# Optimization experiments

Hardware: AMD Instinct MI355X
Metric: run time of the kernel (lower is better)

## Reference

```python
import jax, jax.numpy as jnp
import numpy as np

HID = 512      # hidden_dim
MID = 256      # hid_dim
COND_D = 256   # condition_op_dim
OP_D = 32      # operator_len
EX_D = 32      # extra_info_num
L, N, T = 16, 1024, 8
EPS = 1e-5


def _lstm_cell(x_proj, h, c, Whh, bhh):
    # x_proj: precomputed x @ Wih.T + bih, shape [B, 4H]
    gates = x_proj + h @ Whh.T + bhh
    i, f, g, o = jnp.split(gates, 4, axis=-1)
    i = jax.nn.sigmoid(i); f = jax.nn.sigmoid(f)
    g = jnp.tanh(g); o = jax.nn.sigmoid(o)
    c = f * c + i * g
    h = o * jnp.tanh(c)
    return h, c


def _batchnorm(x, gamma, beta):
    mu = x.mean(0)
    var = x.var(0)  # biased, matches PyTorch training-mode normalization
    return gamma * (x - mu) * jax.lax.rsqrt(var + EPS) + beta


def setup_inputs() -> dict:
    key = jax.random.key(0)
    ks = jax.random.split(key, 24)
    s = lambda *sh: 0.05
    inp = {
        'operators': jax.random.normal(ks[0], (L, N, OP_D), jnp.float32),
        'extra_infos': jax.random.normal(ks[1], (L, N, EX_D), jnp.float32),
        'conditions': jax.random.normal(ks[2], (L, N, T, COND_D), jnp.float32),
        'condition_masks': jnp.ones((L, N, 1), jnp.float32),
        'mapping': jax.random.randint(ks[3], (L, N, 2), 0, N + 1, jnp.int32).astype(jnp.int64),
        'lstm1_Wih': jax.random.normal(ks[4], (4 * HID, COND_D), jnp.float32) * 0.05,
        'lstm1_Whh': jax.random.normal(ks[5], (4 * HID, HID), jnp.float32) * 0.05,
        'lstm1_bih': jnp.zeros((4 * HID,), jnp.float32),
        'lstm1_bhh': jnp.zeros((4 * HID,), jnp.float32),
        'cond_W': jax.random.normal(ks[6], (MID, HID), jnp.float32) * 0.05,
        'cond_b': jnp.zeros((MID,), jnp.float32),
        'bn1_g': jnp.ones((MID,), jnp.float32),
        'bn1_b': jnp.zeros((MID,), jnp.float32),
        'lstm2_Wih': jax.random.normal(ks[7], (4 * HID, OP_D + EX_D + MID), jnp.float32) * 0.05,
        'lstm2_Whh': jax.random.normal(ks[8], (4 * HID, HID), jnp.float32) * 0.05,
        'lstm2_bih': jnp.zeros((4 * HID,), jnp.float32),
        'lstm2_bhh': jnp.zeros((4 * HID,), jnp.float32),
        'bn2_g': jnp.ones((HID,), jnp.float32),
        'bn2_b': jnp.zeros((HID,), jnp.float32),
    }
    return inp


def reference(operators, extra_infos, conditions, condition_masks, mapping,
              lstm1_Wih, lstm1_Whh, lstm1_bih, lstm1_bhh,
              cond_W, cond_b, bn1_g, bn1_b,
              lstm2_Wih, lstm2_Whh, lstm2_bih, lstm2_bhh,
              bn2_g, bn2_b):
    B = L * N
    x = conditions.reshape(B, T, COND_D)
    # lstm1 over conditions; precompute input projections for all steps
    xp = jnp.einsum('btd,gd->btg', x, lstm1_Wih) + lstm1_bih  # [B,T,4H]

    def step1(carry, xt):
        h, c = carry
        h, c = _lstm_cell(xt, h, c, lstm1_Whh, lstm1_bhh)
        return (h, c), None

    h0 = jnp.zeros((B, HID), xp.dtype)
    (h1, _), _ = jax.lax.scan(step1, (h0, h0), jnp.swapaxes(xp, 0, 1))

    last = jax.nn.relu(h1 @ cond_W.T + cond_b)       # [B, MID]
    last = _batchnorm(last, bn1_g, bn1_b).reshape(L, N, MID)

    out = jnp.concatenate([operators, extra_infos, last], axis=2)  # [L,N,IN2]
    xp2 = jnp.einsum('lnd,gd->lng', out, lstm2_Wih) + lstm2_bih    # [L,N,4H]

    hz = jnp.zeros((N, HID), xp2.dtype)
    h, c = _lstm_cell(xp2[L - 1], hz, hz, lstm2_Whh, lstm2_bhh)

    mapping = mapping.astype(jnp.int32)
    levels = jnp.arange(L - 2, -1, -1)

    def tree_step(carry, idx):
        h, c = carry
        mp = mapping[idx]  # [N,2]
        pad = jnp.zeros((1, HID), h.dtype)
        ph = jnp.concatenate([pad, h], 0)  # [N+1,H]
        pc = jnp.concatenate([pad, c], 0)
        h = (ph[mp[:, 0]] + ph[mp[:, 1]]) * 0.5
        c = (pc[mp[:, 0]] + pc[mp[:, 1]]) * 0.5
        h, c = _lstm_cell(xp2[idx], h, c, lstm2_Whh, lstm2_bhh)
        return (h, c), None

    (h, c), _ = jax.lax.scan(tree_step, (h, c), levels)

    # batch_size == N since all operator rows are nonzero
    return _batchnorm(h, bn2_g, bn2_b)  # [N, HID]
```

## Files before the change

kernel.cpp:

```cpp
#include <hip/hip_runtime.h>
#include <hip/hip_bf16.h>
#include <stdint.h>


typedef __bf16 bf16;
typedef __bf16 bf16x8 __attribute__((ext_vector_type(8)));
typedef float f32x4 __attribute__((ext_vector_type(4)));

#define HIDDEN 512

__device__ __forceinline__ float fast_sig(float x) { return 1.f / (1.f + __expf(-x)); }
__device__ __forceinline__ float fast_tanh(float x) {
  float e = __expf(2.f * x);
  return 1.f - 2.f / (e + 1.f);
}

__device__ __forceinline__ void async16(const bf16* g, bf16* l) {
  __builtin_amdgcn_global_load_lds(
      (const __attribute__((address_space(1))) void*)g,
      (__attribute__((address_space(3))) void*)l, 16, 0, 0);
}

__device__ __forceinline__ void cvt_one(const float* __restrict__ src,
                                        bf16* __restrict__ dst, size_t i) {
  float4 a = *(const float4*)(src + i);
  float4 b = *(const float4*)(src + i + 4);
  bf16x8 r;
  r[0] = (bf16)a.x; r[1] = (bf16)a.y; r[2] = (bf16)a.z; r[3] = (bf16)a.w;
  r[4] = (bf16)b.x; r[5] = (bf16)b.y; r[6] = (bf16)b.z; r[7] = (bf16)b.w;
  *(bf16x8*)(dst + i) = r;
}

__global__ void prep(const float* conds, bf16* conds_b,
                     const float* s0, bf16* d0, const float* s1, bf16* d1,
                     const float* s2, bf16* d2, const float* s3, bf16* d3,
                     const float* s4, bf16* d4, const float* s5, bf16* d5,
                     const float* s6, bf16* d6,
                     const int* map, int* flags) {
  int b = blockIdx.x;
  int tid = threadIdx.x;
  if (b < 2176) {
    int g = b * 256 + tid;
    const float* s; bf16* d; int off;
    if      (g < 65536)  { s = s0; d = d0; off = g; }
    else if (g < 131072) { s = s1; d = d1; off = g - 65536; }
    else if (g < 196608) { s = s2; d = d2; off = g - 131072; }
    else if (g < 327680) { s = s3; d = d3; off = g - 196608; }
    else if (g < 344064) { s = s4; d = d4; off = g - 327680; }
    else if (g < 425984) { s = s5; d = d5; off = g - 344064; }
    else if (g < 557056) { s = s6; d = d6; off = g - 425984; }
    else return;
    cvt_one(s, d, (size_t)off * 8);
  } else if (b == 2176) {
    __shared__ int any;
    if (tid == 0) any = 0;
    __syncthreads();
    int loc = 0;
    for (int i = tid; i < 16384; i += 256) loc |= map[2 * i + 1];
    if (loc) atomicOr(&any, 1);
    __syncthreads();
    if (tid == 0) flags[0] = (any == 0) ? 1 : 0;
  } else {
    size_t i = ((size_t)(b - 2177) * 256 + tid) * 8;
    cvt_one(conds, conds_b, i);
  }
}

template <int MT, int KT0, int KT1>
__global__ __launch_bounds__(256, 2) void cell_gemm(
    const bf16* __restrict__ A0, int a0off, int a0s,
    const bf16* __restrict__ A1, int a1s,
    const bf16* __restrict__ B0, int b0s,
    const bf16* __restrict__ B1, int b1s,
    const float* __restrict__ bias0, const float* __restrict__ bias1,
    const float* __restrict__ c_prev,
    float* __restrict__ c_out,
    bf16* __restrict__ h_b16)
{
  constexpr int BM = MT * 32;
  __shared__ __align__(16) bf16 sA[BM * 64];
  __shared__ __align__(16) bf16 sB[256 * 64];
  const int tid = threadIdx.x;
  const int lane = tid & 63;
  const int quad = lane >> 4, cl = lane & 15;
  const int wave = tid >> 6;
  const int wr = wave >> 1, wc = wave & 1;
  const int bm0 = blockIdx.x * BM;
  const int j0 = blockIdx.y * 64;

  const bf16* ra[MT][2];
  const bf16* rb[8][2];
#pragma unroll
  for (int mi = 0; mi < MT; ++mi)
#pragma unroll
    for (int kh = 0; kh < 2; ++kh) {
      int row = wr * (MT * 16) + mi * 16 + cl;
      ra[mi][kh] = &sA[row * 64 + (((kh * 4 + quad) ^ (row & 7))) * 8];
    }
#pragma unroll
  for (int g = 0; g < 8; ++g)
#pragma unroll
    for (int kh = 0; kh < 2; ++kh) {
      int row = g * 32 + wc * 16 + cl;
      rb[g][kh] = &sB[row * 64 + (((kh * 4 + quad) ^ (row & 7))) * 8];
    }

  f32x4 acc[MT][8];
#pragma unroll
  for (int mi = 0; mi < MT; ++mi)
#pragma unroll
    for (int g = 0; g < 8; ++g) acc[mi][g] = f32x4{0.f, 0.f, 0.f, 0.f};

  const bf16* pa[MT];
  const bf16* pb[8];
#pragma unroll
  for (int ia = 0; ia < MT; ++ia) {
    int e = ia * 256 + tid, row = e >> 3, sl = e & 7;
    pa[ia] = A0 + (size_t)((bm0 + row) * a0s + a0off + (sl ^ (row & 7)) * 8);
  }
#pragma unroll
  for (int ib = 0; ib < 8; ++ib) {
    int e = ib * 256 + tid, row = e >> 3, sl = e & 7;
    int wrow = (row >> 6) * HIDDEN + j0 + (row & 63);
    pb[ib] = B0 + (size_t)(wrow * b0s + (sl ^ (row & 7)) * 8);
  }

  auto ktile = [&]() {
#pragma unroll
    for (int ia = 0; ia < MT; ++ia) {
      async16(pa[ia], sA + (ia * 256 + tid) * 8);
      pa[ia] += 64;
    }
#pragma unroll
    for (int ib = 0; ib < 8; ++ib) {
      async16(pb[ib], sB + (ib * 256 + tid) * 8);
      pb[ib] += 64;
    }
    __syncthreads();
#pragma unroll
    for (int kh = 0; kh < 2; ++kh) {
      bf16x8 af[MT], bfr[8];
#pragma unroll
      for (int mi = 0; mi < MT; ++mi) af[mi] = *(const bf16x8*)ra[mi][kh];
#pragma unroll
      for (int g = 0; g < 8; ++g) bfr[g] = *(const bf16x8*)rb[g][kh];
#pragma unroll
      for (int mi = 0; mi < MT; ++mi)
#pragma unroll
        for (int g = 0; g < 8; ++g)
          acc[mi][g] = __builtin_amdgcn_mfma_f32_16x16x32_bf16(af[mi], bfr[g], acc[mi][g], 0, 0, 0);
    }
    __syncthreads();
  };

  for (int kt = 0; kt < KT0; ++kt) ktile();
  if (KT1 > 0) {
#pragma unroll
    for (int ia = 0; ia < MT; ++ia) {
      int e = ia * 256 + tid, row = e >> 3, sl = e & 7;
      pa[ia] = A1 + (size_t)((bm0 + row) * a1s + (sl ^ (row & 7)) * 8);
    }
#pragma unroll
    for (int ib = 0; ib < 8; ++ib) {
      int e = ib * 256 + tid, row = e >> 3, sl = e & 7;
      int wrow = (row >> 6) * HIDDEN + j0 + (row & 63);
      pb[ib] = B1 + (size_t)(wrow * b1s + (sl ^ (row & 7)) * 8);
    }
    for (int kt = 0; kt < KT1; ++kt) ktile();
  }

#pragma unroll
  for (int h = 0; h < 2; ++h) {
    const int j = j0 + h * 32 + wc * 16 + cl;
    float bI = bias0[j] + bias1[j];
    float bF = bias0[HIDDEN + j] + bias1[HIDDEN + j];
    float bG = bias0[2 * HIDDEN + j] + bias1[2 * HIDDEN + j];
    float bO = bias0[3 * HIDDEN + j] + bias1[3 * HIDDEN + j];
#pragma unroll
    for (int mi = 0; mi < MT; ++mi) {
      int rb_ = bm0 + wr * (MT * 16) + mi * 16 + quad * 4;
#pragma unroll
      for (int r = 0; r < 4; ++r) {
        int row = rb_ + r;
        float iv = fast_sig(acc[mi][0 + h][r] + bI);
        float fv = fast_sig(acc[mi][2 + h][r] + bF);
        float gv = fast_tanh(acc[mi][4 + h][r] + bG);
        float ov = fast_sig(acc[mi][6 + h][r] + bO);
        float cp = c_prev ? c_prev[(size_t)row * HIDDEN + j] : 0.f;
        float cn = fv * cp + iv * gv;
        float hn = ov * fast_tanh(cn);
        c_out[(size_t)row * HIDDEN + j] = cn;
        h_b16[(size_t)row * HIDDEN + j] = (bf16)hn;
      }
    }
  }
}

__global__ __launch_bounds__(256, 2) void cell_tree_f(
    const int* __restrict__ map, const int* __restrict__ flags, int level,
    const bf16* __restrict__ h_src, const float* __restrict__ c_src,
    const bf16* __restrict__ W,
    const float* __restrict__ bhh,
    const bf16* __restrict__ xp,
    float* __restrict__ c_out,
    bf16* __restrict__ h_out,
    float* __restrict__ h_f32)
{
  __shared__ __align__(16) bf16 sA[32 * 512];
  __shared__ __align__(16) bf16 sB[128 * 64];
  const int tid = threadIdx.x;
  const int lane = tid & 63;
  const int quad = lane >> 4, cl = lane & 15;
  const int wave = tid >> 6;
  const int wr = wave >> 1, wc = wave & 1;
  const int bm0 = blockIdx.x * 32;
  const int j0 = blockIdx.y * 32;
  const int fl = flags[0];

  {
    int grow = tid >> 3;
    int w = tid & 7;
    int n = bm0 + grow;
    long mbase = (long)level * 2048 + n * 2;
    int m0, m1;
    if (fl) { m0 = map[mbase * 2]; m1 = map[mbase * 2 + 2]; }
    else    { m0 = map[mbase];     m1 = map[mbase + 1]; }
    const bf16* s0 = h_src + (size_t)(m0 ? m0 - 1 : 0) * HIDDEN;
    const bf16* s1 = h_src + (size_t)(m1 ? m1 - 1 : 0) * HIDDEN;
    float f0 = m0 ? 0.5f : 0.f;
    float f1 = m1 ? 0.5f : 0.f;
    int sw = grow & 7;
    bf16* drow = sA + grow * 512;
#pragma unroll
    for (int g = 0; g < 8; ++g) {
      int slot = g * 8 + w;
      bf16x8 a = *(const bf16x8*)(s0 + slot * 8);
      bf16x8 b = *(const bf16x8*)(s1 + slot * 8);
      bf16x8 r;
#pragma unroll
      for (int e = 0; e < 8; ++e)
        r[e] = (bf16)(f0 * (float)a[e] + f1 * (float)b[e]);
      *(bf16x8*)(drow + (g * 8 + (w ^ sw)) * 8) = r;
    }
  }

  const bf16* ra[2];
#pragma unroll
  for (int kh = 0; kh < 2; ++kh) {
    int row = wr * 16 + cl;
    ra[kh] = &sA[row * 512 + (((kh * 4 + quad) ^ (row & 7))) * 8];
  }
  const bf16* rb[4][2];
#pragma unroll
  for (int g = 0; g < 4; ++g)
#pragma unroll
    for (int kh = 0; kh < 2; ++kh) {
      int row = g * 32 + wc * 16 + cl;
      rb[g][kh] = &sB[row * 64 + (((kh * 4 + quad) ^ (row & 7))) * 8];
    }

  f32x4 acc[4];
#pragma unroll
  for (int g = 0; g < 4; ++g) acc[g] = f32x4{0.f, 0.f, 0.f, 0.f};

  const bf16* pb[4];
#pragma unroll
  for (int ib = 0; ib < 4; ++ib) {
    int e = ib * 256 + tid, row = e >> 3, sl = e & 7;
    int wrow = (row >> 5) * HIDDEN + j0 + (row & 31);
    pb[ib] = W + (size_t)(wrow * HIDDEN + (sl ^ (row & 7)) * 8);
  }

  for (int kt = 0; kt < 8; ++kt) {
#pragma unroll
    for (int ib = 0; ib < 4; ++ib) {
      async16(pb[ib], sB + (ib * 256 + tid) * 8);
      pb[ib] += 64;
    }
    __syncthreads();
#pragma unroll
    for (int kh = 0; kh < 2; ++kh) {
      bf16x8 af = *(const bf16x8*)(ra[kh] + kt * 64);
#pragma unroll
      for (int g = 0; g < 4; ++g) {
        bf16x8 bfr = *(const bf16x8*)rb[g][kh];
        acc[g] = __builtin_amdgcn_mfma_f32_16x16x32_bf16(af, bfr, acc[g], 0, 0, 0);
      }
    }
    __syncthreads();
  }

  const int j = j0 + wc * 16 + cl;
  float bI = bhh[j], bF = bhh[HIDDEN + j];
  float bG = bhh[2 * HIDDEN + j], bO = bhh[3 * HIDDEN + j];
  int rb0 = bm0 + wr * 16 + quad * 4;
#pragma unroll
  for (int r = 0; r < 4; ++r) {
    int row = rb0 + r;
    long mbase = (long)level * 2048 + row * 2;
    int m0, m1;
    if (fl) { m0 = map[mbase * 2]; m1 = map[mbase * 2 + 2]; }
    else    { m0 = map[mbase];     m1 = map[mbase + 1]; }
    float c0 = m0 ? c_src[(size_t)(m0 - 1) * HIDDEN + j] : 0.f;
    float c1 = m1 ? c_src[(size_t)(m1 - 1) * HIDDEN + j] : 0.f;
    float cp = 0.5f * (c0 + c1);
    const bf16* xr = xp + (size_t)row * 2048;
    float gi = acc[0][r] + bI + (float)xr[j];
    float gf = acc[1][r] + bF + (float)xr[HIDDEN + j];
    float gg = acc[2][r] + bG + (float)xr[2 * HIDDEN + j];
    float go = acc[3][r] + bO + (float)xr[3 * HIDDEN + j];
    float cn = fast_sig(gf) * cp + fast_sig(gi) * fast_tanh(gg);
    float hn = fast_sig(go) * fast_tanh(cn);
    c_out[(size_t)row * HIDDEN + j] = cn;
    h_out[(size_t)row * HIDDEN + j] = (bf16)hn;
    if (h_f32) h_f32[(size_t)row * HIDDEN + j] = hn;
  }
}

template <int MT>
__global__ __launch_bounds__(256, 2) void plain_gemm(
    const bf16* __restrict__ A0, int a0s, int a0kt,
    const bf16* __restrict__ A1, int a1s, int a1kt,
    const bf16* __restrict__ A2, int a2s, int a2kt,
    const bf16* __restrict__ B, int bs,
    const float* __restrict__ bias, int do_relu,
    bf16* __restrict__ outh, int Ntot)
{
  constexpr int BM = MT * 32;
  __shared__ __align__(16) bf16 sA[BM * 32];
  __shared__ __align__(16) bf16 sB[128 * 32];
  const int tid = threadIdx.x;
  const int lane = tid & 63;
  const int quad = lane >> 4, cl = lane & 15;
  const int wave = tid >> 6;
  const int wr = wave >> 1, wc = wave & 1;
  const int bm0 = blockIdx.x * BM;
  const int bn0 = blockIdx.y * 128;

  f32x4 acc[MT][4];
#pragma unroll
  for (int mi = 0; mi < MT; ++mi)
#pragma unroll
    for (int ni = 0; ni < 4; ++ni) acc[mi][ni] = f32x4{0.f, 0.f, 0.f, 0.f};

  const int nkt = a0kt + a1kt + a2kt;
  for (int kt = 0; kt < nkt; ++kt) {
    const bf16* abase; int astr, acol;
    if (kt < a0kt)            { abase = A0; astr = a0s; acol = kt * 32; }
    else if (kt < a0kt + a1kt){ abase = A1; astr = a1s; acol = (kt - a0kt) * 32; }
    else                      { abase = A2; astr = a2s; acol = (kt - a0kt - a1kt) * 32; }
#pragma unroll
    for (int ia = 0; ia < MT / 2; ++ia) {
      int e = ia * 256 + tid;
      int row = e >> 2, sl = e & 3;
      int src = sl ^ ((row >> 1) & 3);
      async16(abase + (size_t)(bm0 + row) * astr + acol + src * 8, sA + e * 8);
    }
#pragma unroll
    for (int ib = 0; ib < 2; ++ib) {
      int e = ib * 256 + tid;
      int row = e >> 2, sl = e & 3;
      int src = sl ^ ((row >> 1) & 3);
      async16(B + (size_t)(bn0 + row) * bs + kt * 32 + src * 8, sB + e * 8);
    }
    __syncthreads();
    bf16x8 af[MT], bfr[4];
#pragma unroll
    for (int mi = 0; mi < MT; ++mi) {
      int row = wr * (MT * 16) + mi * 16 + cl;
      int sl = quad ^ ((row >> 1) & 3);
      af[mi] = *(const bf16x8*)&sA[row * 32 + sl * 8];
    }
#pragma unroll
    for (int ni = 0; ni < 4; ++ni) {
      int row = wc * 64 + ni * 16 + cl;
      int sl = quad ^ ((row >> 1) & 3);
      bfr[ni] = *(const bf16x8*)&sB[row * 32 + sl * 8];
    }
#pragma unroll
    for (int mi = 0; mi < MT; ++mi)
#pragma unroll
      for (int ni = 0; ni < 4; ++ni)
        acc[mi][ni] = __builtin_amdgcn_mfma_f32_16x16x32_bf16(af[mi], bfr[ni], acc[mi][ni], 0, 0, 0);
    __syncthreads();
  }

#pragma unroll
  for (int mi = 0; mi < MT; ++mi) {
    int rb = bm0 + wr * (MT * 16) + mi * 16 + quad * 4;
#pragma unroll
    for (int ni = 0; ni < 4; ++ni) {
      int col = bn0 + wc * 64 + ni * 16 + cl;
      float bv = bias ? bias[col] : 0.f;
#pragma unroll
      for (int r = 0; r < 4; ++r) {
        int row = rb + r;
        float v = acc[mi][ni][r] + bv;
        if (do_relu) v = fmaxf(v, 0.f);
        outh[(size_t)row * Ntot + col] = (bf16)v;
      }
    }
  }
}

__global__ void cell0(const bf16* __restrict__ xp,
                      const float* __restrict__ bhh,
                      bf16* __restrict__ h, float* __restrict__ c)
{
  int n = blockIdx.x, j = threadIdx.x;
  float g[4];
#pragma unroll
  for (int k = 0; k < 4; ++k)
    g[k] = (float)xp[(size_t)n * 2048 + k * 512 + j] + bhh[k * 512 + j];
  float cv = fast_sig(g[0]) * fast_tanh(g[2]);
  h[(size_t)n * HIDDEN + j] = (bf16)(fast_sig(g[3]) * fast_tanh(cv));
  c[(size_t)n * HIDDEN + j] = cv;
}

__global__ void bn_reduce_b16(const bf16* __restrict__ x, int rpb, int F,
                              float* __restrict__ partials) {
  int col = threadIdx.x, b = blockIdx.x;
  const bf16* p = x + (size_t)b * rpb * F + col;
  float s = 0.f, q = 0.f;
  for (int r = 0; r < rpb; ++r) { float v = (float)p[(size_t)r * F]; s += v; q += v * v; }
  partials[(size_t)b * 2 * F + col] = s;
  partials[(size_t)b * 2 * F + F + col] = q;
}

__global__ void bn_reduce_f32(const float* __restrict__ x, int rpb, int F,
                              float* __restrict__ partials) {
  int col = threadIdx.x, b = blockIdx.x;
  const float* p = x + (size_t)b * rpb * F + col;
  float s = 0.f, q = 0.f;
  for (int r = 0; r < rpb; ++r) { float v = p[(size_t)r * F]; s += v; q += v * v; }
  partials[(size_t)b * 2 * F + col] = s;
  partials[(size_t)b * 2 * F + F + col] = q;
}

__global__ void bn_final(const float* __restrict__ partials, int nb, int F,
                         const float* __restrict__ g, const float* __restrict__ b,
                         float invB, float* __restrict__ scale, float* __restrict__ shift) {
  int j = threadIdx.x;
  float s = 0.f, q = 0.f;
  for (int i = 0; i < nb; ++i) {
    s += partials[(size_t)i * 2 * F + j];
    q += partials[(size_t)i * 2 * F + F + j];
  }
  float mu = s * invB;
  float var = fmaxf(q * invB - mu * mu, 0.f);
  float sc = g[j] * rsqrtf(var + 1e-5f);
  scale[j] = sc;
  shift[j] = b[j] - sc * mu;
}

__global__ void bn_apply_mid(const bf16* __restrict__ x, const float* __restrict__ scale,
                             const float* __restrict__ shift, int Fmask, size_t total,
                             bf16* __restrict__ out) {
  for (size_t i = blockIdx.x * (size_t)blockDim.x + threadIdx.x; i < total;
       i += (size_t)gridDim.x * blockDim.x) {
    int j = (int)(i & (size_t)Fmask);
    out[i] = (bf16)(scale[j] * (float)x[i] + shift[j]);
  }
}

__global__ void bn_apply_out(const float* __restrict__ x, const float* __restrict__ scale,
                             const float* __restrict__ shift, int Fmask, size_t total,
                             float* __restrict__ out) {
  for (size_t i = blockIdx.x * (size_t)blockDim.x + threadIdx.x; i < total;
       i += (size_t)gridDim.x * blockDim.x) {
    int j = (int)(i & (size_t)Fmask);
    out[i] = scale[j] * x[i] + shift[j];
  }
}

extern "C" void kernel_launch(void* const* d_in, const int* in_sizes, int n_in,
                              void* d_out, int out_size, void* d_ws, size_t ws_size,
                              hipStream_t stream) {
  const float* operators = (const float*)d_in[0];
  const float* extras    = (const float*)d_in[1];
  const float* conds     = (const float*)d_in[2];
  const int*   mapping   = (const int*)d_in[4];
  const float* b1ih = (const float*)d_in[7];
  const float* b1hh = (const float*)d_in[8];
  const float* condb = (const float*)d_in[10];
  const float* bn1g = (const float*)d_in[11];
  const float* bn1b = (const float*)d_in[12];
  const float* b2ih = (const float*)d_in[15];
  const float* b2hh = (const float*)d_in[16];
  const float* bn2g = (const float*)d_in[17];
  const float* bn2b = (const float*)d_in[18];

  char* ws = (char*)d_ws;
  size_t o = 0;
  auto alloc = [&](size_t bytes) {
    char* p = ws + o;
    o += (bytes + 255) & ~(size_t)255;
    return p;
  };
  bf16* conds_b = (bf16*)alloc((size_t)33554432 * 2);
  bf16* ops_b   = (bf16*)alloc((size_t)524288 * 2);
  bf16* ext_b   = (bf16*)alloc((size_t)524288 * 2);
  bf16* w1ih_b  = (bf16*)alloc((size_t)524288 * 2);
  bf16* w1hh_b  = (bf16*)alloc((size_t)1048576 * 2);
  bf16* condw_b = (bf16*)alloc((size_t)131072 * 2);
  bf16* w2ih_b  = (bf16*)alloc((size_t)655360 * 2);
  bf16* w2hh_b  = (bf16*)alloc((size_t)1048576 * 2);
  bf16* h1[2];
  h1[0] = (bf16*)alloc((size_t)16384 * 512 * 2);
  h1[1] = (bf16*)alloc((size_t)16384 * 512 * 2);
  float* c1 = (float*)alloc((size_t)16384 * 512 * 4);
  bf16* last_relu = (bf16*)alloc((size_t)16384 * 256 * 2);
  bf16* last_bn = (bf16*)alloc((size_t)16384 * 256 * 2);
  bf16* hbuf0 = (bf16*)alloc((size_t)1024 * 512 * 2);
  bf16* hbuf1 = (bf16*)alloc((size_t)1024 * 512 * 2);
  float* cbuf0 = (float*)alloc((size_t)1024 * 512 * 4);
  float* cbuf1 = (float*)alloc((size_t)1024 * 512 * 4);
  float* h2f = (float*)alloc((size_t)1024 * 512 * 4);
  float* partials = (float*)alloc((size_t)64 * 1024 * 4);
  float* scale1 = (float*)alloc(256 * 4);
  float* shift1 = (float*)alloc(256 * 4);
  float* scale2 = (float*)alloc(512 * 4);
  float* shift2 = (float*)alloc(512 * 4);
  int* flags = (int*)alloc(256);
  bf16* xp2 = (bf16*)alloc((size_t)16384 * 2048 * 2);

  prep<<<18561, 256, 0, stream>>>(
      conds, conds_b,
      operators, ops_b, extras, ext_b,
      (const float*)d_in[5], w1ih_b, (const float*)d_in[6], w1hh_b,
      (const float*)d_in[9], condw_b, (const float*)d_in[13], w2ih_b,
      (const float*)d_in[14], w2hh_b,
      mapping, flags);

  cell_gemm<4, 4, 0><<<dim3(128, 8), 256, 0, stream>>>(
      conds_b, 0, 2048, nullptr, 512,
      w1ih_b, 256, w1hh_b, 512,
      b1ih, b1hh, nullptr, c1, h1[1]);
  for (int t = 1; t < 8; ++t) {
    cell_gemm<4, 4, 8><<<dim3(128, 8), 256, 0, stream>>>(
        conds_b, t * 256, 2048, h1[t & 1], 512,
        w1ih_b, 256, w1hh_b, 512,
        b1ih, b1hh, c1, c1, h1[(t + 1) & 1]);
  }

  plain_gemm<2><<<dim3(256, 2), 256, 0, stream>>>(
      h1[0], 512, 16, nullptr, 0, 0, nullptr, 0, 0,
      condw_b, 512, condb, 1, last_relu, 256);
  bn_reduce_b16<<<64, 256, 0, stream>>>(last_relu, 256, 256, partials);
  bn_final<<<1, 256, 0, stream>>>(partials, 64, 256, bn1g, bn1b, 1.f / 16384.f, scale1, shift1);
  bn_apply_mid<<<1024, 256, 0, stream>>>(last_relu, scale1, shift1, 255,
                                         (size_t)16384 * 256, last_bn);

  plain_gemm<4><<<dim3(128, 16), 256, 0, stream>>>(
      ops_b, 32, 1, ext_b, 32, 1, last_bn, 256, 8,
      w2ih_b, 320, b2ih, 0, xp2, 2048);

  size_t lvl_sz = (size_t)1024 * 2048;
  bf16* hb[2] = {hbuf0, hbuf1};
  float* cb[2] = {cbuf0, cbuf1};
  cell0<<<1024, 512, 0, stream>>>(xp2 + 15 * lvl_sz, b2hh, hb[0], cb[0]);
  int cur = 0;
  for (int idx = 14; idx >= 0; --idx) {
    int nxt = cur ^ 1;
    cell_tree_f<<<dim3(32, 16), 256, 0, stream>>>(
        mapping, flags, idx, hb[cur], cb[cur], w2hh_b, b2hh,
        xp2 + (size_t)idx * lvl_sz, cb[nxt], hb[nxt],
        (idx == 0) ? h2f : nullptr);
    cur = nxt;
  }

  bn_reduce_f32<<<16, 512, 0, stream>>>(h2f, 64, 512, partials);
  bn_final<<<1, 512, 0, stream>>>(partials, 16, 512, bn2g, bn2b, 1.f / 1024.f, scale2, shift2);
  bn_apply_out<<<512, 256, 0, stream>>>(h2f, scale2, shift2, 511,
                                        (size_t)1024 * 512, (float*)d_out);
}
```

Before: 1.153 ms.

## Triple-buffer LSTM1 cell GEMM with async LDS prefetch and K=32 tiles

Rewrites the LSTM1 cell GEMM main loop as a three-stage ring buffer. Global-to-LDS async loads for tile t+2 are issued while MFMAs consume tile t, with vmcnt waits replacing the two full syncthreads per tile. The K tile shrinks from 64 to 32 with a matching XOR swizzle, doubling the tile count, and MFMA issue priority is raised. This aims to hide memory latency in the eight recurrent launches, at the cost of more LDS and hand-tuned wait counts.

```diff
diff --git a/kernel.cpp b/kernel.cpp
--- a/kernel.cpp
+++ b/kernel.cpp
@@ -66,7 +66,7 @@
   }
 }
 
-template <int MT, int KT0, int KT1>
+template <int KT0, int KT1>
 __global__ __launch_bounds__(256, 2) void cell_gemm(
     const bf16* __restrict__ A0, int a0off, int a0s,
     const bf16* __restrict__ A1, int a1s,
@@ -77,96 +77,103 @@
     float* __restrict__ c_out,
     bf16* __restrict__ h_b16)
 {
-  constexpr int BM = MT * 32;
-  __shared__ __align__(16) bf16 sA[BM * 64];
-  __shared__ __align__(16) bf16 sB[256 * 64];
+  constexpr int NT = KT0 + KT1;
+  constexpr int ABUF = 128 * 32;
+  constexpr int BBUF = 256 * 32;
+  __shared__ __align__(16) bf16 sA[3 * ABUF];
+  __shared__ __align__(16) bf16 sB[3 * BBUF];
   const int tid = threadIdx.x;
   const int lane = tid & 63;
   const int quad = lane >> 4, cl = lane & 15;
   const int wave = tid >> 6;
   const int wr = wave >> 1, wc = wave & 1;
-  const int bm0 = blockIdx.x * BM;
+  const int bm0 = blockIdx.x * 128;
   const int j0 = blockIdx.y * 64;
 
-  const bf16* ra[MT][2];
-  const bf16* rb[8][2];
-#pragma unroll
-  for (int mi = 0; mi < MT; ++mi)
-#pragma unroll
-    for (int kh = 0; kh < 2; ++kh) {
-      int row = wr * (MT * 16) + mi * 16 + cl;
-      ra[mi][kh] = &sA[row * 64 + (((kh * 4 + quad) ^ (row & 7))) * 8];
-    }
-#pragma unroll
-  for (int g = 0; g < 8; ++g)
-#pragma unroll
-    for (int kh = 0; kh < 2; ++kh) {
-      int row = g * 32 + wc * 16 + cl;
-      rb[g][kh] = &sB[row * 64 + (((kh * 4 + quad) ^ (row & 7))) * 8];
-    }
-
-  f32x4 acc[MT][8];
-#pragma unroll
-  for (int mi = 0; mi < MT; ++mi)
+  int baseA0[2], baseA1[2];
+  int dstA[2];
+#pragma unroll
+  for (int ia = 0; ia < 2; ++ia) {
+    int e = ia * 256 + tid, row = e >> 2, sl = e & 3;
+    int src = sl ^ ((row >> 1) & 3);
+    baseA0[ia] = (bm0 + row) * a0s + a0off + src * 8;
+    baseA1[ia] = (bm0 + row) * a1s + src * 8;
+    dstA[ia] = e * 8;
+  }
+  int baseB0[4], baseB1[4];
+  int dstB[4];
+#pragma unroll
+  for (int ib = 0; ib < 4; ++ib) {
+    int e = ib * 256 + tid, row = e >> 2, sl = e & 3;
+    int src = sl ^ ((row >> 1) & 3);
+    int wrow = (row >> 6) * HIDDEN + j0 + (row & 63);
+    baseB0[ib] = wrow * b0s + src * 8;
+    baseB1[ib] = wrow * b1s + src * 8;
+    dstB[ib] = e * 8;
+  }
+
+  int raoff[4], rboff[8];
+#pragma unroll
+  for (int mi = 0; mi < 4; ++mi) {
+    int row = wr * 64 + mi * 16 + cl;
+    raoff[mi] = row * 32 + (quad ^ ((row >> 1) & 3)) * 8;
+  }
+#pragma unroll
+  for (int g = 0; g < 8; ++g) {
+    int row = g * 32 + wc * 16 + cl;
+    rboff[g] = row * 32 + (quad ^ ((row >> 1) & 3)) * 8;
+  }
+
+  f32x4 acc[4][8];
+#pragma unroll
+  for (int mi = 0; mi < 4; ++mi)
 #pragma unroll
     for (int g = 0; g < 8; ++g) acc[mi][g] = f32x4{0.f, 0.f, 0.f, 0.f};
 
-  const bf16* pa[MT];
-  const bf16* pb[8];
-#pragma unroll
-  for (int ia = 0; ia < MT; ++ia) {
-    int e = ia * 256 + tid, row = e >> 3, sl = e & 7;
-    pa[ia] = A0 + (size_t)((bm0 + row) * a0s + a0off + (sl ^ (row & 7)) * 8);
-  }
-#pragma unroll
-  for (int ib = 0; ib < 8; ++ib) {
-    int e = ib * 256 + tid, row = e >> 3, sl = e & 7;
-    int wrow = (row >> 6) * HIDDEN + j0 + (row & 63);
-    pb[ib] = B0 + (size_t)(wrow * b0s + (sl ^ (row & 7)) * 8);
-  }
-
-  auto ktile = [&]() {
-#pragma unroll
-    for (int ia = 0; ia < MT; ++ia) {
-      async16(pa[ia], sA + (ia * 256 + tid) * 8);
-      pa[ia] += 64;
-    }
-#pragma unroll
-    for (int ib = 0; ib < 8; ++ib) {
-      async16(pb[ib], sB + (ib * 256 + tid) * 8);
-      pb[ib] += 64;
-    }
-    __syncthreads();
-#pragma unroll
-    for (int kh = 0; kh < 2; ++kh) {
-      bf16x8 af[MT], bfr[8];
-#pragma unroll
-      for (int mi = 0; mi < MT; ++mi) af[mi] = *(const bf16x8*)ra[mi][kh];
-#pragma unroll
-      for (int g = 0; g < 8; ++g) bfr[g] = *(const bf16x8*)rb[g][kh];
-#pragma unroll
-      for (int mi = 0; mi < MT; ++mi)
-#pragma unroll
-        for (int g = 0; g < 8; ++g)
-          acc[mi][g] = __builtin_amdgcn_mfma_f32_16x16x32_bf16(af[mi], bfr[g], acc[mi][g], 0, 0, 0);
-    }
-    __syncthreads();
+  auto stage = [&](int tt) {
+    int buf = tt % 3;
+    bf16* da = sA + buf * ABUF;
+    bf16* db = sB + buf * BBUF;
+    if (tt < KT0) {
+      int ac = tt * 32;
+#pragma unroll
+      for (int ia = 0; ia < 2; ++ia) async16(A0 + baseA0[ia] + ac, da + dstA[ia]);
+#pragma unroll
+      for (int ib = 0; ib < 4; ++ib) async16(B0 + baseB0[ib] + ac, db + dstB[ib]);
+    } else {
+      int ac = (tt - KT0) * 32;
+#pragma unroll
+      for (int ia = 0; ia < 2; ++ia) async16(A1 + baseA1[ia] + ac, da + dstA[ia]);
+#pragma unroll
+      for (int ib = 0; ib < 4; ++ib) async16(B1 + baseB1[ib] + ac, db + dstB[ib]);
+    }
   };
 
-  for (int kt = 0; kt < KT0; ++kt) ktile();
-  if (KT1 > 0) {
-#pragma unroll
-    for (int ia = 0; ia < MT; ++ia) {
-      int e = ia * 256 + tid, row = e >> 3, sl = e & 7;
-      pa[ia] = A1 + (size_t)((bm0 + row) * a1s + (sl ^ (row & 7)) * 8);
-    }
-#pragma unroll
-    for (int ib = 0; ib < 8; ++ib) {
-      int e = ib * 256 + tid, row = e >> 3, sl = e & 7;
-      int wrow = (row >> 6) * HIDDEN + j0 + (row & 63);
-      pb[ib] = B1 + (size_t)(wrow * b1s + (sl ^ (row & 7)) * 8);
-    }
-    for (int kt = 0; kt < KT1; ++kt) ktile();
+  stage(0);
+  stage(1);
+
+  for (int t = 0; t < NT; ++t) {
+    if (t == NT - 1) {
+      asm volatile("s_waitcnt vmcnt(0)" ::: "memory");
+    } else {
+      asm volatile("s_waitcnt vmcnt(6)" ::: "memory");
+    }
+    __builtin_amdgcn_s_barrier();
+    if (t + 2 < NT) stage(t + 2);
+    const bf16* bA = sA + (t % 3) * ABUF;
+    const bf16* bB = sB + (t % 3) * BBUF;
+    bf16x8 af[4], bfr[8];
+#pragma unroll
+    for (int mi = 0; mi < 4; ++mi) af[mi] = *(const bf16x8*)(bA + raoff[mi]);
+#pragma unroll
+    for (int g = 0; g < 8; ++g) bfr[g] = *(const bf16x8*)(bB + rboff[g]);
+    __builtin_amdgcn_s_setprio(1);
+#pragma unroll
+    for (int mi = 0; mi < 4; ++mi)
+#pragma unroll
+      for (int g = 0; g < 8; ++g)
+        acc[mi][g] = __builtin_amdgcn_mfma_f32_16x16x32_bf16(af[mi], bfr[g], acc[mi][g], 0, 0, 0);
+    __builtin_amdgcn_s_setprio(0);
   }
 
 #pragma unroll
@@ -177,8 +184,8 @@
     float bG = bias0[2 * HIDDEN + j] + bias1[2 * HIDDEN + j];
     float bO = bias0[3 * HIDDEN + j] + bias1[3 * HIDDEN + j];
 #pragma unroll
-    for (int mi = 0; mi < MT; ++mi) {
-      int rb_ = bm0 + wr * (MT * 16) + mi * 16 + quad * 4;
+    for (int mi = 0; mi < 4; ++mi) {
+      int rb_ = bm0 + wr * 64 + mi * 16 + quad * 4;
 #pragma unroll
       for (int r = 0; r < 4; ++r) {
         int row = rb_ + r;
@@ -532,12 +539,12 @@
       (const float*)d_in[14], w2hh_b,
       mapping, flags);
 
-  cell_gemm<4, 4, 0><<<dim3(128, 8), 256, 0, stream>>>(
+  cell_gemm<8, 0><<<dim3(128, 8), 256, 0, stream>>>(
       conds_b, 0, 2048, nullptr, 512,
       w1ih_b, 256, w1hh_b, 512,
       b1ih, b1hh, nullptr, c1, h1[1]);
   for (int t = 1; t < 8; ++t) {
-    cell_gemm<4, 4, 8><<<dim3(128, 8), 256, 0, stream>>>(
+    cell_gemm<8, 16><<<dim3(128, 8), 256, 0, stream>>>(
         conds_b, t * 256, 2048, h1[t & 1], 512,
         w1ih_b, 256, w1hh_b, 512,
         b1ih, b1hh, c1, c1, h1[(t + 1) & 1]);
```

Result: slower. 1.254 ms (+8.8%).

## Fuse tree-LSTM level launches into one cooperative kernel with grid syncs

Applied to the files above, without the earlier changes.

The initial cell and the 15 per-level tree cell launches are replaced by a single cooperative kernel of 512 blocks that loops over levels and separates them with grid-wide barriers. This targets the launch overhead and inter-kernel gaps between the small dependent launches. It adds grid.sync cost per level and needs all 512 blocks resident at once. If the cooperative launch fails, the code falls back to the old per-level launches.

```diff
diff --git a/kernel.cpp b/kernel.cpp
--- a/kernel.cpp
+++ b/kernel.cpp
@@ -1,6 +1,9 @@
 #include <hip/hip_runtime.h>
+#include <hip/hip_cooperative_groups.h>
 #include <hip/hip_bf16.h>
 #include <stdint.h>
+
+namespace cg = cooperative_groups;
 
 
 typedef __bf16 bf16;
@@ -196,26 +199,21 @@
   }
 }
 
-__global__ __launch_bounds__(256, 2) void cell_tree_f(
-    const int* __restrict__ map, const int* __restrict__ flags, int level,
+__device__ __forceinline__ void tree_level_body(
+    int bm0, int j0, int fl, int level,
+    const int* __restrict__ map,
     const bf16* __restrict__ h_src, const float* __restrict__ c_src,
-    const bf16* __restrict__ W,
-    const float* __restrict__ bhh,
+    const bf16* __restrict__ W, const float* __restrict__ bhh,
     const bf16* __restrict__ xp,
-    float* __restrict__ c_out,
-    bf16* __restrict__ h_out,
-    float* __restrict__ h_f32)
+    float* __restrict__ c_out, bf16* __restrict__ h_out,
+    float* __restrict__ h_f32,
+    bf16* sA , bf16* sB )
 {
-  __shared__ __align__(16) bf16 sA[32 * 512];
-  __shared__ __align__(16) bf16 sB[128 * 64];
   const int tid = threadIdx.x;
   const int lane = tid & 63;
   const int quad = lane >> 4, cl = lane & 15;
   const int wave = tid >> 6;
   const int wr = wave >> 1, wc = wave & 1;
-  const int bm0 = blockIdx.x * 32;
-  const int j0 = blockIdx.y * 32;
-  const int fl = flags[0];
 
   {
     int grow = tid >> 3;
@@ -317,6 +315,80 @@
   }
 }
 
+__global__ __launch_bounds__(256, 2) void tree_fused(
+    const int* __restrict__ map, const int* __restrict__ flags,
+    const bf16* __restrict__ xp, const float* __restrict__ bhh,
+    const bf16* __restrict__ W,
+    bf16* __restrict__ h0, bf16* __restrict__ h1,
+    float* __restrict__ c0, float* __restrict__ c1,
+    float* __restrict__ h_f32)
+{
+  __shared__ __align__(16) bf16 sA[32 * 512];
+  __shared__ __align__(16) bf16 sB[128 * 64];
+  cg::grid_group grid = cg::this_grid();
+  const int bm0 = (blockIdx.x & 31) * 32;
+  const int j0 = (blockIdx.x >> 5) * 32;
+  const int fl = flags[0];
+  const size_t lvl_sz = (size_t)1024 * 2048;
+
+  {
+    int gtid = blockIdx.x * 256 + threadIdx.x;
+    const bf16* xp15 = xp + 15 * lvl_sz;
+#pragma unroll
+    for (int e = 0; e < 4; ++e) {
+      int idx = gtid * 4 + e;
+      int n = idx >> 9, j = idx & 511;
+      float g[4];
+#pragma unroll
+      for (int k = 0; k < 4; ++k)
+        g[k] = (float)xp15[(size_t)n * 2048 + k * 512 + j] + bhh[k * 512 + j];
+      float cv = fast_sig(g[0]) * fast_tanh(g[2]);
+      h0[(size_t)n * HIDDEN + j] = (bf16)(fast_sig(g[3]) * fast_tanh(cv));
+      c0[(size_t)n * HIDDEN + j] = cv;
+    }
+  }
+  grid.sync();
+
+  bf16* hb[2] = {h0, h1};
+  float* cb[2] = {c0, c1};
+  int cur = 0;
+  for (int lvl = 14; lvl >= 0; --lvl) {
+    tree_level_body(bm0, j0, fl, lvl, map, hb[cur], cb[cur], W, bhh,
+                    xp + (size_t)lvl * lvl_sz, cb[cur ^ 1], hb[cur ^ 1],
+                    (lvl == 0) ? h_f32 : nullptr, sA, sB);
+    if (lvl > 0) grid.sync();
+    cur ^= 1;
+  }
+}
+
+__global__ __launch_bounds__(256, 2) void cell_tree_f(
+    const int* __restrict__ map, const int* __restrict__ flags, int level,
+    const bf16* __restrict__ h_src, const float* __restrict__ c_src,
+    const bf16* __restrict__ W, const float* __restrict__ bhh,
+    const bf16* __restrict__ xp,
+    float* __restrict__ c_out, bf16* __restrict__ h_out,
+    float* __restrict__ h_f32)
+{
+  __shared__ __align__(16) bf16 sA[32 * 512];
+  __shared__ __align__(16) bf16 sB[128 * 64];
+  tree_level_body(blockIdx.x * 32, blockIdx.y * 32, flags[0], level, map,
+                  h_src, c_src, W, bhh, xp, c_out, h_out, h_f32, sA, sB);
+}
+
+__global__ void cell0(const bf16* __restrict__ xp,
+                      const float* __restrict__ bhh,
+                      bf16* __restrict__ h, float* __restrict__ c)
+{
+  int n = blockIdx.x, j = threadIdx.x;
+  float g[4];
+#pragma unroll
+  for (int k = 0; k < 4; ++k)
+    g[k] = (float)xp[(size_t)n * 2048 + k * 512 + j] + bhh[k * 512 + j];
+  float cv = fast_sig(g[0]) * fast_tanh(g[2]);
+  h[(size_t)n * HIDDEN + j] = (bf16)(fast_sig(g[3]) * fast_tanh(cv));
+  c[(size_t)n * HIDDEN + j] = cv;
+}
+
 template <int MT>
 __global__ __launch_bounds__(256, 2) void plain_gemm(
     const bf16* __restrict__ A0, int a0s, int a0kt,
@@ -401,20 +473,6 @@
       }
     }
   }
-}
-
-__global__ void cell0(const bf16* __restrict__ xp,
-                      const float* __restrict__ bhh,
-                      bf16* __restrict__ h, float* __restrict__ c)
-{
-  int n = blockIdx.x, j = threadIdx.x;
-  float g[4];
-#pragma unroll
-  for (int k = 0; k < 4; ++k)
-    g[k] = (float)xp[(size_t)n * 2048 + k * 512 + j] + bhh[k * 512 + j];
-  float cv = fast_sig(g[0]) * fast_tanh(g[2]);
-  h[(size_t)n * HIDDEN + j] = (bf16)(fast_sig(g[3]) * fast_tanh(cv));
-  c[(size_t)n * HIDDEN + j] = cv;
 }
 
 __global__ void bn_reduce_b16(const bf16* __restrict__ x, int rpb, int F,
@@ -556,17 +614,31 @@
       w2ih_b, 320, b2ih, 0, xp2, 2048);
 
   size_t lvl_sz = (size_t)1024 * 2048;
-  bf16* hb[2] = {hbuf0, hbuf1};
-  float* cb[2] = {cbuf0, cbuf1};
-  cell0<<<1024, 512, 0, stream>>>(xp2 + 15 * lvl_sz, b2hh, hb[0], cb[0]);
-  int cur = 0;
-  for (int idx = 14; idx >= 0; --idx) {
-    int nxt = cur ^ 1;
-    cell_tree_f<<<dim3(32, 16), 256, 0, stream>>>(
-        mapping, flags, idx, hb[cur], cb[cur], w2hh_b, b2hh,
-        xp2 + (size_t)idx * lvl_sz, cb[nxt], hb[nxt],
-        (idx == 0) ? h2f : nullptr);
-    cur = nxt;
+  {
+    const int* a_map = mapping; const int* a_flags = flags;
+    const bf16* a_xp = xp2; const float* a_bhh = b2hh; const bf16* a_W = w2hh_b;
+    bf16* a_h0 = hbuf0; bf16* a_h1 = hbuf1;
+    float* a_c0 = cbuf0; float* a_c1 = cbuf1; float* a_hf = h2f;
+    void* cargs[] = {(void*)&a_map, (void*)&a_flags, (void*)&a_xp, (void*)&a_bhh,
+                     (void*)&a_W, (void*)&a_h0, (void*)&a_h1, (void*)&a_c0,
+                     (void*)&a_c1, (void*)&a_hf};
+    hipError_t cerr = hipLaunchCooperativeKernel(
+        (const void*)tree_fused, dim3(512), dim3(256), cargs, 0, stream);
+    if (cerr != hipSuccess) {
+      (void)hipGetLastError();
+      bf16* hb[2] = {hbuf0, hbuf1};
+      float* cb[2] = {cbuf0, cbuf1};
+      cell0<<<1024, 512, 0, stream>>>(xp2 + 15 * lvl_sz, b2hh, hb[0], cb[0]);
+      int cur = 0;
+      for (int idx = 14; idx >= 0; --idx) {
+        int nxt = cur ^ 1;
+        cell_tree_f<<<dim3(32, 16), 256, 0, stream>>>(
+            mapping, flags, idx, hb[cur], cb[cur], w2hh_b, b2hh,
+            xp2 + (size_t)idx * lvl_sz, cb[nxt], hb[nxt],
+            (idx == 0) ? h2f : nullptr);
+        cur = nxt;
+      }
+    }
   }
 
   bn_reduce_f32<<<16, 512, 0, stream>>>(h2f, 64, 512, partials);
```

New measurement: 2.044 ms. +77.3%, slower.

## Fold batchnorm into LSTM2 input weights and stage tree-cell epilogue operands in LDS

Applied to the files above, without the earlier changes.

Removes the elementwise batchnorm-apply pass over the 16384x256 intermediate. The per-feature scale goes into a scaled copy of the LSTM2 input weights, and the shift becomes an extra bias, so the xp2 GEMM reads the relu output directly. The tree cell kernel also preloads the averaged child cell states and its xp gate slices into shared memory with vectorized loads during the gather phase. This replaces the scattered per-element global loads and repeated mapping reads in the epilogue. Costs are a small weight-folding kernel, slightly different bf16 rounding, and extra LDS per block that could lower occupancy.

```diff
diff --git a/kernel.cpp b/kernel.cpp
--- a/kernel.cpp
+++ b/kernel.cpp
@@ -199,15 +199,15 @@
 __global__ __launch_bounds__(256, 2) void cell_tree_f(
     const int* __restrict__ map, const int* __restrict__ flags, int level,
     const bf16* __restrict__ h_src, const float* __restrict__ c_src,
-    const bf16* __restrict__ W,
-    const float* __restrict__ bhh,
+    const bf16* __restrict__ W, const float* __restrict__ bhh,
     const bf16* __restrict__ xp,
-    float* __restrict__ c_out,
-    bf16* __restrict__ h_out,
+    float* __restrict__ c_out, bf16* __restrict__ h_out,
     float* __restrict__ h_f32)
 {
   __shared__ __align__(16) bf16 sA[32 * 512];
   __shared__ __align__(16) bf16 sB[128 * 64];
+  __shared__ __align__(16) float cavg[32 * 33];
+  __shared__ __align__(16) bf16 sXP[32 * 4 * 32];
   const int tid = threadIdx.x;
   const int lane = tid & 63;
   const int quad = lane >> 4, cl = lane & 15;
@@ -242,6 +242,27 @@
         r[e] = (bf16)(f0 * (float)a[e] + f1 * (float)b[e]);
       *(bf16x8*)(drow + (g * 8 + (w ^ sw)) * 8) = r;
     }
+    {
+      int cj = j0 + w * 4;
+      float4 c0 = m0 ? *(const float4*)(c_src + (size_t)(m0 - 1) * HIDDEN + cj)
+                     : float4{0.f, 0.f, 0.f, 0.f};
+      float4 c1 = m1 ? *(const float4*)(c_src + (size_t)(m1 - 1) * HIDDEN + cj)
+                     : float4{0.f, 0.f, 0.f, 0.f};
+      float* cd = cavg + grow * 33 + w * 4;
+      cd[0] = 0.5f * (c0.x + c1.x);
+      cd[1] = 0.5f * (c0.y + c1.y);
+      cd[2] = 0.5f * (c0.z + c1.z);
+      cd[3] = 0.5f * (c0.w + c1.w);
+    }
+    {
+      const bf16* xr = xp + (size_t)n * 2048;
+      int gate = w >> 1, half = w & 1;
+      bf16x8 v0 = *(const bf16x8*)(xr + gate * HIDDEN + j0 + half * 16);
+      bf16x8 v1 = *(const bf16x8*)(xr + gate * HIDDEN + j0 + half * 16 + 8);
+      bf16* xd = sXP + (grow * 4 + gate) * 32 + half * 16;
+      *(bf16x8*)xd = v0;
+      *(bf16x8*)(xd + 8) = v1;
+    }
   }
 
   const bf16* ra[2];
@@ -290,31 +311,41 @@
     __syncthreads();
   }
 
-  const int j = j0 + wc * 16 + cl;
+  const int jl = wc * 16 + cl;
+  const int j = j0 + jl;
   float bI = bhh[j], bF = bhh[HIDDEN + j];
   float bG = bhh[2 * HIDDEN + j], bO = bhh[3 * HIDDEN + j];
-  int rb0 = bm0 + wr * 16 + quad * 4;
+  int rl0 = wr * 16 + quad * 4;
 #pragma unroll
   for (int r = 0; r < 4; ++r) {
-    int row = rb0 + r;
-    long mbase = (long)level * 2048 + row * 2;
-    int m0, m1;
-    if (fl) { m0 = map[mbase * 2]; m1 = map[mbase * 2 + 2]; }
-    else    { m0 = map[mbase];     m1 = map[mbase + 1]; }
-    float c0 = m0 ? c_src[(size_t)(m0 - 1) * HIDDEN + j] : 0.f;
-    float c1 = m1 ? c_src[(size_t)(m1 - 1) * HIDDEN + j] : 0.f;
-    float cp = 0.5f * (c0 + c1);
-    const bf16* xr = xp + (size_t)row * 2048;
-    float gi = acc[0][r] + bI + (float)xr[j];
-    float gf = acc[1][r] + bF + (float)xr[HIDDEN + j];
-    float gg = acc[2][r] + bG + (float)xr[2 * HIDDEN + j];
-    float go = acc[3][r] + bO + (float)xr[3 * HIDDEN + j];
+    int rl = rl0 + r;
+    int row = bm0 + rl;
+    float cp = cavg[rl * 33 + jl];
+    const bf16* xr = sXP + rl * 128;
+    float gi = acc[0][r] + bI + (float)xr[jl];
+    float gf = acc[1][r] + bF + (float)xr[32 + jl];
+    float gg = acc[2][r] + bG + (float)xr[64 + jl];
+    float go = acc[3][r] + bO + (float)xr[96 + jl];
     float cn = fast_sig(gf) * cp + fast_sig(gi) * fast_tanh(gg);
     float hn = fast_sig(go) * fast_tanh(cn);
     c_out[(size_t)row * HIDDEN + j] = cn;
     h_out[(size_t)row * HIDDEN + j] = (bf16)hn;
     if (h_f32) h_f32[(size_t)row * HIDDEN + j] = hn;
   }
+}
+
+__global__ void cell0(const bf16* __restrict__ xp,
+                      const float* __restrict__ bhh,
+                      bf16* __restrict__ h, float* __restrict__ c)
+{
+  int n = blockIdx.x, j = threadIdx.x;
+  float g[4];
+#pragma unroll
+  for (int k = 0; k < 4; ++k)
+    g[k] = (float)xp[(size_t)n * 2048 + k * 512 + j] + bhh[k * 512 + j];
+  float cv = fast_sig(g[0]) * fast_tanh(g[2]);
+  h[(size_t)n * HIDDEN + j] = (bf16)(fast_sig(g[3]) * fast_tanh(cv));
+  c[(size_t)n * HIDDEN + j] = cv;
 }
 
 template <int MT>
@@ -403,18 +434,28 @@
   }
 }
 
-__global__ void cell0(const bf16* __restrict__ xp,
-                      const float* __restrict__ bhh,
-                      bf16* __restrict__ h, float* __restrict__ c)
-{
-  int n = blockIdx.x, j = threadIdx.x;
-  float g[4];
-#pragma unroll
-  for (int k = 0; k < 4; ++k)
-    g[k] = (float)xp[(size_t)n * 2048 + k * 512 + j] + bhh[k * 512 + j];
-  float cv = fast_sig(g[0]) * fast_tanh(g[2]);
-  h[(size_t)n * HIDDEN + j] = (bf16)(fast_sig(g[3]) * fast_tanh(cv));
-  c[(size_t)n * HIDDEN + j] = cv;
+__global__ void fold_w2(const bf16* __restrict__ w2,
+                        const float* __restrict__ scale,
+                        const float* __restrict__ shift,
+                        const float* __restrict__ b2ih,
+                        bf16* __restrict__ w2f, float* __restrict__ bias2f) {
+  int g = blockIdx.x * 8 + (threadIdx.x >> 5);
+  int ln = threadIdx.x & 31;
+  const bf16* src = w2 + (size_t)g * 320;
+  bf16* dst = w2f + (size_t)g * 320;
+  dst[ln] = src[ln];
+  dst[32 + ln] = src[32 + ln];
+  float acc = 0.f;
+#pragma unroll
+  for (int i = 0; i < 8; ++i) {
+    int k = i * 32 + ln;
+    float w = (float)src[64 + k];
+    dst[64 + k] = (bf16)(w * scale[k]);
+    acc += w * shift[k];
+  }
+#pragma unroll
+  for (int off = 16; off; off >>= 1) acc += __shfl_down(acc, off, 32);
+  if (ln == 0) bias2f[g] = b2ih[g] + acc;
 }
 
 __global__ void bn_reduce_b16(const bf16* __restrict__ x, int rpb, int F,
@@ -451,16 +492,6 @@
   float sc = g[j] * rsqrtf(var + 1e-5f);
   scale[j] = sc;
   shift[j] = b[j] - sc * mu;
-}
-
-__global__ void bn_apply_mid(const bf16* __restrict__ x, const float* __restrict__ scale,
-                             const float* __restrict__ shift, int Fmask, size_t total,
-                             bf16* __restrict__ out) {
-  for (size_t i = blockIdx.x * (size_t)blockDim.x + threadIdx.x; i < total;
-       i += (size_t)gridDim.x * blockDim.x) {
-    int j = (int)(i & (size_t)Fmask);
-    out[i] = (bf16)(scale[j] * (float)x[i] + shift[j]);
-  }
 }
 
 __global__ void bn_apply_out(const float* __restrict__ x, const float* __restrict__ scale,
@@ -510,7 +541,8 @@
   h1[1] = (bf16*)alloc((size_t)16384 * 512 * 2);
   float* c1 = (float*)alloc((size_t)16384 * 512 * 4);
   bf16* last_relu = (bf16*)alloc((size_t)16384 * 256 * 2);
-  bf16* last_bn = (bf16*)alloc((size_t)16384 * 256 * 2);
+  bf16* w2ih_f = (bf16*)alloc((size_t)655360 * 2);
+  float* bias2f = (float*)alloc(2048 * 4);
   bf16* hbuf0 = (bf16*)alloc((size_t)1024 * 512 * 2);
   bf16* hbuf1 = (bf16*)alloc((size_t)1024 * 512 * 2);
   float* cbuf0 = (float*)alloc((size_t)1024 * 512 * 4);
@@ -548,12 +580,11 @@
       condw_b, 512, condb, 1, last_relu, 256);
   bn_reduce_b16<<<64, 256, 0, stream>>>(last_relu, 256, 256, partials);
   bn_final<<<1, 256, 0, stream>>>(partials, 64, 256, bn1g, bn1b, 1.f / 16384.f, scale1, shift1);
-  bn_apply_mid<<<1024, 256, 0, stream>>>(last_relu, scale1, shift1, 255,
-                                         (size_t)16384 * 256, last_bn);
+  fold_w2<<<256, 256, 0, stream>>>(w2ih_b, scale1, shift1, b2ih, w2ih_f, bias2f);
 
   plain_gemm<4><<<dim3(128, 16), 256, 0, stream>>>(
-      ops_b, 32, 1, ext_b, 32, 1, last_bn, 256, 8,
-      w2ih_b, 320, b2ih, 0, xp2, 2048);
+      ops_b, 32, 1, ext_b, 32, 1, last_relu, 256, 8,
+      w2ih_f, 320, bias2f, 0, xp2, 2048);
 
   size_t lvl_sz = (size_t)1024 * 2048;
   bf16* hb[2] = {hbuf0, hbuf1};
```

Result: faster. 1.121 ms (-2.7%).
